# Performance work log

Hardware: AMD Instinct MI355X
Metric: run time of the kernel (lower is better)

Reference implementation:

```python
import jax, jax.numpy as jnp
import numpy as np

BETA = 0.05  # module hardcodes self.beta = 0.05 regardless of init arg
K = 4096
D = 512


def setup_inputs() -> dict:
    key = jax.random.key(0)
    k1, k2 = jax.random.split(key)
    latents = jax.random.normal(k1, (32, 1024, D), dtype=jnp.float32)
    # nn.Embedding weight init: normal_(mean=0.8, std=0.1)
    emb_weight = 0.8 + 0.1 * jax.random.normal(k2, (K, D), dtype=jnp.float32)
    return {"latents": latents, "emb_weight": emb_weight}


def reference(latents, emb_weight):
    B, S, Dm = latents.shape
    flat = latents.reshape(-1, Dm)  # [N, D]
    dist = (jnp.sum(flat * flat, axis=1, keepdims=True)
            + jnp.sum(emb_weight * emb_weight, axis=1)
            - 2.0 * jnp.matmul(flat, emb_weight.T))  # [N, K]
    inds = jnp.argmin(dist, axis=1)  # [N]
    quantized = emb_weight[inds].reshape(B, S, Dm)  # gather instead of one-hot matmul

    commitment_loss = jnp.mean((jax.lax.stop_gradient(quantized) - latents) ** 2)
    embedding_loss = jnp.mean((quantized - jax.lax.stop_gradient(latents)) ** 2)
    vq_loss = commitment_loss * BETA + embedding_loss

    # straight-through estimator
    quantized_st = latents + jax.lax.stop_gradient(quantized - latents)

    N = flat.shape[0]
    avg_probs = jnp.zeros((K,), dtype=latents.dtype).at[inds].add(1.0) / N
    perplexity = jnp.exp(-jnp.sum(avg_probs * jnp.log(avg_probs + 1e-10)))

    output_inds = inds.reshape(B, S)
    return (quantized_st, vq_loss, output_inds, emb_weight, perplexity)
```

## Files before the change

kernel.cpp:

```cpp
#include <hip/hip_runtime.h>
#include <cfloat>
#include <cmath>
#include <climits>
#include <cstdint>

#define N_ROWS   32768
#define D_DIM    512
#define K_CODES  4096

#define EPS_GAP  0.008f
#define CAND_WIN 0.02f
#define FLAG_CAP 12000

typedef short s16x8 __attribute__((ext_vector_type(8)));
typedef float f32x4 __attribute__((ext_vector_type(4)));


__device__ __forceinline__ short f2bf_rne(float x) {
    unsigned u = __float_as_uint(x);
    unsigned r = (u + 0x7fffu + ((u >> 16) & 1u)) >> 16;
    return (short)r;
}
__device__ __forceinline__ float bf2f(short b) {
    return __uint_as_float(((unsigned)(unsigned short)b) << 16);
}

__device__ __forceinline__ void gld16(const short* g, short* l) {
    __builtin_amdgcn_global_load_lds(
        reinterpret_cast<const __attribute__((address_space(1))) unsigned int*>(
            reinterpret_cast<uintptr_t>(g)),
        reinterpret_cast<__attribute__((address_space(3))) unsigned int*>(
            (unsigned int)(reinterpret_cast<uintptr_t>(l))),
        16, 0, 0);
}

__device__ __forceinline__ float np_block128_sq(const float* p) {
    float P[16];
    #pragma unroll
    for (int l = 0; l < 16; ++l) {
        float s0 = __fmul_rn(p[0 * 16 + l], p[0 * 16 + l]);
        float s1 = __fmul_rn(p[1 * 16 + l], p[1 * 16 + l]);
        float s2 = __fmul_rn(p[2 * 16 + l], p[2 * 16 + l]);
        float s3 = __fmul_rn(p[3 * 16 + l], p[3 * 16 + l]);
        float s4 = __fmul_rn(p[4 * 16 + l], p[4 * 16 + l]);
        float s5 = __fmul_rn(p[5 * 16 + l], p[5 * 16 + l]);
        float s6 = __fmul_rn(p[6 * 16 + l], p[6 * 16 + l]);
        float s7 = __fmul_rn(p[7 * 16 + l], p[7 * 16 + l]);
        float a01 = __fadd_rn(s0, s1);
        float a23 = __fadd_rn(s2, s3);
        float a45 = __fadd_rn(s4, s5);
        float a67 = __fadd_rn(s6, s7);
        P[l] = __fadd_rn(__fadd_rn(a01, a23), __fadd_rn(a45, a67));
    }
    float T3[8];
    #pragma unroll
    for (int k = 0; k < 8; ++k) T3[k] = __fadd_rn(P[k], P[k + 8]);
    float T6[4];
    #pragma unroll
    for (int k = 0; k < 4; ++k) T6[k] = __fadd_rn(T3[k], T3[k + 4]);
    return __fadd_rn(__fadd_rn(__fadd_rn(T6[0], T6[1]), T6[2]), T6[3]);
}
__device__ __forceinline__ float np_sum512_sq(const float* p) {
    float B0 = np_block128_sq(p);
    float B1 = np_block128_sq(p + 128);
    float B2 = np_block128_sq(p + 256);
    float B3 = np_block128_sq(p + 384);
    return __fadd_rn(__fadd_rn(B0, B1), __fadd_rn(B2, B3));
}

__global__ void vq_convert(const float* __restrict__ lat, const float* __restrict__ emb,
                           short* __restrict__ lat_hi, short* __restrict__ lat_lo,
                           short* __restrict__ emb_hi, short* __restrict__ emb_lo) {
    int i = blockIdx.x * 256 + threadIdx.x;
    const float* src; short *dh, *dl; size_t base;
    if (i < 2097152) { src = lat; dh = lat_hi; dl = lat_lo; base = (size_t)i * 8; }
    else             { src = emb; dh = emb_hi; dl = emb_lo; base = (size_t)(i - 2097152) * 8; }
    float4 a = *(const float4*)(src + base);
    float4 b = *(const float4*)(src + base + 4);
    float x[8] = {a.x, a.y, a.z, a.w, b.x, b.y, b.z, b.w};
    s16x8 hv, lv;
    #pragma unroll
    for (int j = 0; j < 8; ++j) {
        short h = f2bf_rne(x[j]);
        hv[j] = h;
        lv[j] = f2bf_rne(x[j] - bf2f(h));
    }
    *(s16x8*)(dh + base) = hv;
    *(s16x8*)(dl + base) = lv;
}

__global__ void vq_enorm(const float* __restrict__ emb, float* __restrict__ e_norm) {
    int item = blockIdx.x * 4 + (threadIdx.x >> 6);
    int lane = threadIdx.x & 63;
    const float4* s4 = (const float4*)(emb + (size_t)item * D_DIM);
    float4 a = s4[lane];
    float4 b = s4[64 + lane];
    float s = a.x * a.x + a.y * a.y + a.z * a.z + a.w * a.w
            + b.x * b.x + b.y * b.y + b.z * b.z + b.w * b.w;
    #pragma unroll
    for (int off = 32; off > 0; off >>= 1) s += __shfl_down(s, off);
    if (lane == 0) e_norm[item] = s;
}

__device__ __forceinline__ int kswz(int r) { return (r & 3) ^ ((r >> 2) & 3); }

#define BUFS 24576

__global__ __launch_bounds__(512, 2)
void vq_argmin_mfma(const short* __restrict__ Ah_g, const short* __restrict__ Al_g,
                    const short* __restrict__ Bh_g, const short* __restrict__ Bl_g,
                    const float* __restrict__ e_norm,
                    unsigned short* __restrict__ fidx,
                    int* __restrict__ flagcnt, int* __restrict__ flaglist)
{
    __shared__ short smem[2 * BUFS];

    const int tid = threadIdx.x;
    const int l   = tid & 63;
    const int wid = tid >> 6;
    const int wr  = wid >> 2;
    const int wc  = wid & 3;
    const int l15 = l & 15;
    const int lhi = l >> 4;
    const int row0 = blockIdx.x * 128;

    float best[16], sec[16];
    int   bidx[16];
    #pragma unroll
    for (int s = 0; s < 16; ++s) { best[s] = FLT_MAX; sec[s] = FLT_MAX; bidx[s] = 0; }

    int offA[4], offB[4];
    #pragma unroll
    for (int m = 0; m < 4; ++m) {
        int r = wr * 64 + m * 16 + l15;
        offA[m] = r * 32 + (lhi ^ kswz(r)) * 8;
    }
    #pragma unroll
    for (int n = 0; n < 4; ++n) {
        int r = wc * 64 + n * 16 + l15;
        offB[n] = r * 32 + (lhi ^ kswz(r)) * 8;
    }

    const int ar  = tid >> 2, asl = tid & 3;
    const size_t a_go0 = (size_t)(row0 + ar) * D_DIM + (asl ^ kswz(ar)) * 8;

    {
        gld16(Ah_g + a_go0, smem + tid * 8);
        gld16(Al_g + a_go0, smem + 4096 + tid * 8);
        #pragma unroll
        for (int jj = 0; jj < 2; ++jj) {
            int cc = jj * 512 + tid;
            int rr = cc >> 2, sll = cc & 3;
            size_t go = (size_t)rr * D_DIM + (sll ^ kswz(rr)) * 8;
            gld16(Bh_g + go, smem + 8192 + cc * 8);
            gld16(Bl_g + go, smem + 16384 + cc * 8);
        }
    }
    __syncthreads();

    f32x4 acc[4][4];
    #pragma unroll
    for (int m = 0; m < 4; ++m)
        #pragma unroll
        for (int n = 0; n < 4; ++n) acc[m][n] = (f32x4){0.f, 0.f, 0.f, 0.f};

    for (int s = 0; s < 256; ++s) {
        short* cur = smem + (s & 1) * BUFS;

        if (s < 255) {
            const int s1 = s + 1;
            const int k0 = (s1 & 15) * 32;
            const int cb0 = (s1 >> 4) * 256;
            short* nb = smem + ((s1 & 1)) * BUFS;
            gld16(Ah_g + a_go0 + k0, nb + tid * 8);
            gld16(Al_g + a_go0 + k0, nb + 4096 + tid * 8);
            #pragma unroll
            for (int jj = 0; jj < 2; ++jj) {
                int cc = jj * 512 + tid;
                int rr = cc >> 2, sll = cc & 3;
                size_t go = (size_t)(cb0 + rr) * D_DIM + k0 + (sll ^ kswz(rr)) * 8;
                gld16(Bh_g + go, nb + 8192 + cc * 8);
                gld16(Bl_g + go, nb + 16384 + cc * 8);
            }
        }

        s16x8 ah[4], al[4], bh[4], bl[4];
        #pragma unroll
        for (int m = 0; m < 4; ++m) {
            ah[m] = *(const s16x8*)(cur + offA[m]);
            al[m] = *(const s16x8*)(cur + 4096 + offA[m]);
        }
        #pragma unroll
        for (int n = 0; n < 4; ++n) {
            bh[n] = *(const s16x8*)(cur + 8192 + offB[n]);
            bl[n] = *(const s16x8*)(cur + 16384 + offB[n]);
        }

        #pragma unroll
        for (int m = 0; m < 4; ++m)
            #pragma unroll
            for (int n = 0; n < 4; ++n) {
                acc[m][n] = __builtin_amdgcn_mfma_f32_16x16x32_bf16(ah[m], bh[n], acc[m][n], 0, 0, 0);
                acc[m][n] = __builtin_amdgcn_mfma_f32_16x16x32_bf16(ah[m], bl[n], acc[m][n], 0, 0, 0);
                acc[m][n] = __builtin_amdgcn_mfma_f32_16x16x32_bf16(al[m], bh[n], acc[m][n], 0, 0, 0);
            }

        if ((s & 15) == 15) {
            const int cb0 = (s >> 4) * 256;
            #pragma unroll
            for (int n = 0; n < 4; ++n) {
                int c = cb0 + wc * 64 + n * 16 + l15;
                float en = e_norm[c];
                #pragma unroll
                for (int m = 0; m < 4; ++m)
                    #pragma unroll
                    for (int r = 0; r < 4; ++r) {
                        float dv = __fmaf_rn(-2.f, acc[m][n][r], en);
                        int si = m * 4 + r;
                        if (dv < best[si]) { sec[si] = best[si]; best[si] = dv; bidx[si] = c; }
                        else if (dv < sec[si]) sec[si] = dv;
                    }
            }
            #pragma unroll
            for (int m = 0; m < 4; ++m)
                #pragma unroll
                for (int n = 0; n < 4; ++n) acc[m][n] = (f32x4){0.f, 0.f, 0.f, 0.f};
        }

        __syncthreads();
    }

    #pragma unroll
    for (int s = 0; s < 16; ++s) {
        float v = best[s], sc = sec[s];
        int ix = bidx[s];
        #pragma unroll
        for (int off = 8; off > 0; off >>= 1) {
            float v2 = __shfl_xor(v, off);
            float s2 = __shfl_xor(sc, off);
            int   i2 = __shfl_xor(ix, off);
            float ns = fminf(fminf(sc, s2), fmaxf(v, v2));
            if (v2 < v || (v2 == v && i2 < ix)) { v = v2; ix = i2; }
            sc = ns;
        }
        best[s] = v; sec[s] = sc; bidx[s] = ix;
    }

    float* mb = (float*)smem;
    float* ms = mb + 512;
    int*   mi = (int*)(mb + 1024);
    if (l15 == 0) {
        #pragma unroll
        for (int m = 0; m < 4; ++m)
            #pragma unroll
            for (int r = 0; r < 4; ++r) {
                int s = m * 4 + r;
                int rowblk = wr * 64 + m * 16 + lhi * 4 + r;
                mb[wc * 128 + rowblk] = best[s];
                ms[wc * 128 + rowblk] = sec[s];
                mi[wc * 128 + rowblk] = bidx[s];
            }
    }
    __syncthreads();
    if (tid < 128) {
        float B = FLT_MAX, S = FLT_MAX;
        int I = 0;
        #pragma unroll
        for (int w = 0; w < 4; ++w) {
            float b = mb[w * 128 + tid], s = ms[w * 128 + tid];
            int i = mi[w * 128 + tid];
            if (b < B || (b == B && i < I)) { S = fminf(B, s); B = b; I = i; }
            else S = fminf(S, fminf(b, s));
        }
        int row = row0 + tid;
        fidx[row] = (unsigned short)I;
        if (S - B < EPS_GAP) {
            int p = atomicAdd(flagcnt, 1);
            if (p < FLAG_CAP) flaglist[p] = row;
        }
    }
}

#define FIXT 1024
#define NWAV 16
#define MAXC 128

__global__ __launch_bounds__(FIXT)
void vq_fixrow(const float* __restrict__ lat, const float* __restrict__ emb,
               const int* __restrict__ flagcnt, const int* __restrict__ flaglist,
               unsigned short* __restrict__ fidx)
{
    __shared__ float xs[D_DIM];
    __shared__ float dall[K_CODES];
    __shared__ float wmin_s[NWAV];
    __shared__ int   ccnt;
    __shared__ int   cands[MAXC];
    __shared__ float cd32[MAXC];

    const int t    = threadIdx.x;
    const int wave = t >> 6;
    const int lane = t & 63;
    int cnt = *flagcnt;
    if (cnt > FLAG_CAP) cnt = FLAG_CAP;

    for (int f = blockIdx.x; f < cnt; f += gridDim.x) {
        const int row = flaglist[f];
        __syncthreads();
        if (t < D_DIM) xs[t] = lat[(size_t)row * D_DIM + t];
        if (t == 0) ccnt = 0;
        __syncthreads();

        float x8[8];
        #pragma unroll
        for (int q = 0; q < 8; ++q) x8[q] = xs[lane * 8 + q];

        float lmin = FLT_MAX;
        for (int c = wave; c < K_CODES; c += 2 * NWAV) {
            const int c2 = c + NWAV;
            const float4* e4a = (const float4*)(emb + (size_t)c  * D_DIM);
            const float4* e4b = (const float4*)(emb + (size_t)c2 * D_DIM);
            float4 ea0 = e4a[lane * 2], ea1 = e4a[lane * 2 + 1];
            float4 eb0 = e4b[lane * 2], eb1 = e4b[lane * 2 + 1];

            float p0 = x8[0] - ea0.x, p1 = x8[1] - ea0.y;
            float p2 = x8[2] - ea0.z, p3 = x8[3] - ea0.w;
            float p4 = x8[4] - ea1.x, p5 = x8[5] - ea1.y;
            float p6 = x8[6] - ea1.z, p7 = x8[7] - ea1.w;
            float sA = __fmaf_rn(p0, p0, __fmaf_rn(p1, p1, __fmaf_rn(p2, p2, p3 * p3)));
            float sB = __fmaf_rn(p4, p4, __fmaf_rn(p5, p5, __fmaf_rn(p6, p6, p7 * p7)));
            float u = sA + sB;

            float q0 = x8[0] - eb0.x, q1 = x8[1] - eb0.y;
            float q2 = x8[2] - eb0.z, q3 = x8[3] - eb0.w;
            float q4 = x8[4] - eb1.x, q5 = x8[5] - eb1.y;
            float q6 = x8[6] - eb1.z, q7 = x8[7] - eb1.w;
            float tA = __fmaf_rn(q0, q0, __fmaf_rn(q1, q1, __fmaf_rn(q2, q2, q3 * q3)));
            float tB = __fmaf_rn(q4, q4, __fmaf_rn(q5, q5, __fmaf_rn(q6, q6, q7 * q7)));
            float v = tA + tB;

            #pragma unroll
            for (int off = 32; off > 0; off >>= 1) {
                u += __shfl_xor(u, off);
                v += __shfl_xor(v, off);
            }
            if (lane == 0) { dall[c] = u; dall[c2] = v; }
            lmin = fminf(lmin, fminf(u, v));
        }
        if (lane == 0) wmin_s[wave] = lmin;
        __syncthreads();

        float gmin = wmin_s[0];
        #pragma unroll
        for (int w = 1; w < NWAV; ++w) gmin = fminf(gmin, wmin_s[w]);
        const float thr = gmin + CAND_WIN;

        for (int c = t; c < K_CODES; c += FIXT) {
            if (dall[c] < thr) {
                int p = atomicAdd(&ccnt, 1);
                if (p < MAXC) cands[p] = c;
            }
        }
        __syncthreads();

        int nc = ccnt < MAXC ? ccnt : MAXC;
        if (t < nc) {
            int c = cands[t];
            const float* e = emb + (size_t)c * D_DIM;
            float t1 = np_sum512_sq(xs);
            float t2 = np_sum512_sq(e);
            float dot = 0.f;
            for (int k = 0; k < D_DIM; ++k)
                dot = __fmaf_rn(xs[k], e[k], dot);
            cd32[t] = __fsub_rn(__fadd_rn(t1, t2), __fmul_rn(2.f, dot));
        }
        __syncthreads();

        if (t == 0) {
            float bv = cd32[0]; int bx = cands[0];
            for (int w = 1; w < nc; ++w)
                if (cd32[w] < bv || (cd32[w] == bv && cands[w] < bx)) {
                    bv = cd32[w]; bx = cands[w];
                }
            fidx[row] = (unsigned short)bx;
        }
    }
}

__global__ void vq_gather(const float* __restrict__ lat, const float* __restrict__ emb,
                          const unsigned short* __restrict__ fidx,
                          float* __restrict__ out_q,
                          float* __restrict__ rowpart, int* __restrict__ hist) {
    int row  = blockIdx.x * 4 + (threadIdx.x >> 6);
    int lane = threadIdx.x & 63;
    int idx  = fidx[row];

    if (lane == 0) atomicAdd(&hist[idx], 1);

    const float4* e4 = (const float4*)(emb + (size_t)idx * D_DIM);
    const float4* x4 = (const float4*)(lat + (size_t)row * D_DIM);
    float4*       q4 = (float4*)(out_q + (size_t)row * D_DIM);

    float s = 0.f;
    #pragma unroll
    for (int i = 0; i < 2; ++i) {
        float4 e = e4[i * 64 + lane];
        float4 x = x4[i * 64 + lane];
        q4[i * 64 + lane] = e;
        float dx = e.x - x.x, dy = e.y - x.y, dz = e.z - x.z, dw = e.w - x.w;
        s += dx * dx + dy * dy + dz * dz + dw * dw;
    }
    #pragma unroll
    for (int off = 32; off > 0; off >>= 1) s += __shfl_down(s, off);
    if (lane == 0) rowpart[row] = s;
}

__global__ void vq_finalize(const float* __restrict__ rowpart, const int* __restrict__ hist,
                            float* __restrict__ out_loss, float* __restrict__ out_perp) {
    __shared__ float sdata[256];
    int t = threadIdx.x;

    float s = 0.f;
    for (int i = t; i < N_ROWS; i += 256) s += rowpart[i];
    sdata[t] = s;
    __syncthreads();
    for (int st = 128; st > 0; st >>= 1) {
        if (t < st) sdata[t] += sdata[t + st];
        __syncthreads();
    }
    if (t == 0) out_loss[0] = 1.05f * (sdata[0] / ((float)N_ROWS * (float)D_DIM));
    __syncthreads();

    float p = 0.f;
    for (int i = t; i < K_CODES; i += 256) {
        float pr = (float)hist[i] / (float)N_ROWS;
        p += pr * logf(pr + 1e-10f);
    }
    sdata[t] = p;
    __syncthreads();
    for (int st = 128; st > 0; st >>= 1) {
        if (t < st) sdata[t] += sdata[t + st];
        __syncthreads();
    }
    if (t == 0) out_perp[0] = expf(-sdata[0]);
}

__global__ void vq_inds(const unsigned short* __restrict__ fidx, float* __restrict__ out_inds) {
    int i = blockIdx.x * 1024 + threadIdx.x;
    out_inds[i] = (float)fidx[i];
}

extern "C" void kernel_launch(void* const* d_in, const int* in_sizes, int n_in,
                              void* d_out, int out_size, void* d_ws, size_t ws_size,
                              hipStream_t stream) {
    const float* lat = (const float*)d_in[0];
    const float* emb = (const float*)d_in[1];
    float* ob = (float*)d_out;

    short* emb_hi = (short*)(ob + 0);
    short* emb_lo = (short*)(ob + 1048576);
    short* lat_hi = (short*)(ob + 2097152);
    short* lat_lo = (short*)(ob + 10485760);
    float* e_norm = ob + 18874368;
    int*   flagcnt  = (int*)(ob + 18878464);
    int*   flaglist = (int*)(ob + 18878465);
    unsigned short* fidx = (unsigned short*)(ob + 18890496);
    int*   hist    = (int*)(ob + 16777220);
    float* rowpart = ob + 16781316;

    float* out_q    = ob;
    float* out_loss = ob + 16777216;
    float* out_inds = ob + 16777217;
    float* out_emb  = ob + 16809985;
    float* out_perp = ob + 18907137;

    hipMemsetAsync(flagcnt, 0, sizeof(int), stream);

    vq_convert<<<dim3(9216), dim3(256), 0, stream>>>(lat, emb, lat_hi, lat_lo, emb_hi, emb_lo);
    vq_enorm<<<dim3(1024), dim3(256), 0, stream>>>(emb, e_norm);

    vq_argmin_mfma<<<dim3(256), dim3(512), 0, stream>>>(lat_hi, lat_lo, emb_hi, emb_lo,
                                                        e_norm, fidx, flagcnt, flaglist);

    hipMemsetAsync(hist, 0, K_CODES * sizeof(int), stream);

    vq_fixrow<<<dim3(512), dim3(FIXT), 0, stream>>>(lat, emb, flagcnt, flaglist, fidx);

    vq_gather<<<dim3(N_ROWS / 4), dim3(256), 0, stream>>>(lat, emb, fidx, out_q, rowpart, hist);

    vq_finalize<<<dim3(1), dim3(256), 0, stream>>>(rowpart, hist, out_loss, out_perp);

    vq_inds<<<dim3(32), dim3(1024), 0, stream>>>(fidx, out_inds);

    hipMemcpyAsync(out_emb, emb, (size_t)K_CODES * D_DIM * sizeof(float),
                   hipMemcpyDeviceToDevice, stream);
}
```

Before: 845.9 us.

## Fuse latent bf16 split into argmin GEMM and split codebook across two blocks

Stops writing hi/lo bf16 copies of the latents to global memory. The argmin kernel now loads fp32 latents and splits them into hi/lo in registers while the next tile is prefetched. The tile grows to 256 rows with 1024 threads, and the codebook is split into two halves along a second grid dimension, followed by a small select kernel that merges the partial minima and flags close calls. Per-row running best/second values move from registers into shared memory and are updated after a shuffle reduction. This removes a large conversion pass and its traffic, at the cost of extra LDS traffic, more synchronisation, and occupancy pressure from the larger block.

```diff
diff --git a/kernel.cpp b/kernel.cpp
--- a/kernel.cpp
+++ b/kernel.cpp
@@ -68,15 +68,12 @@
     return __fadd_rn(__fadd_rn(B0, B1), __fadd_rn(B2, B3));
 }
 
-__global__ void vq_convert(const float* __restrict__ lat, const float* __restrict__ emb,
-                           short* __restrict__ lat_hi, short* __restrict__ lat_lo,
+__global__ void vq_convert(const float* __restrict__ emb,
                            short* __restrict__ emb_hi, short* __restrict__ emb_lo) {
     int i = blockIdx.x * 256 + threadIdx.x;
-    const float* src; short *dh, *dl; size_t base;
-    if (i < 2097152) { src = lat; dh = lat_hi; dl = lat_lo; base = (size_t)i * 8; }
-    else             { src = emb; dh = emb_hi; dl = emb_lo; base = (size_t)(i - 2097152) * 8; }
-    float4 a = *(const float4*)(src + base);
-    float4 b = *(const float4*)(src + base + 4);
+    size_t base = (size_t)i * 8;
+    float4 a = *(const float4*)(emb + base);
+    float4 b = *(const float4*)(emb + base + 4);
     float x[8] = {a.x, a.y, a.z, a.w, b.x, b.y, b.z, b.w};
     s16x8 hv, lv;
     #pragma unroll
@@ -85,8 +82,8 @@
         hv[j] = h;
         lv[j] = f2bf_rne(x[j] - bf2f(h));
     }
-    *(s16x8*)(dh + base) = hv;
-    *(s16x8*)(dl + base) = lv;
+    *(s16x8*)(emb_hi + base) = hv;
+    *(s16x8*)(emb_lo + base) = lv;
 }
 
 __global__ void vq_enorm(const float* __restrict__ emb, float* __restrict__ e_norm) {
@@ -104,16 +101,21 @@
 
 __device__ __forceinline__ int kswz(int r) { return (r & 3) ^ ((r >> 2) & 3); }
 
-#define BUFS 24576
-
-__global__ __launch_bounds__(512, 2)
-void vq_argmin_mfma(const short* __restrict__ Ah_g, const short* __restrict__ Al_g,
+#define BROWS 256
+#define BCOLS 256
+#define KHALF 2048
+#define BUFS2 32768
+
+__global__ __launch_bounds__(1024, 4)
+void vq_argmin_mfma(const float* __restrict__ lat,
                     const short* __restrict__ Bh_g, const short* __restrict__ Bl_g,
                     const float* __restrict__ e_norm,
-                    unsigned short* __restrict__ fidx,
-                    int* __restrict__ flagcnt, int* __restrict__ flaglist)
+                    float* __restrict__ pmin, unsigned short* __restrict__ pidx16)
 {
-    __shared__ short smem[2 * BUFS];
+    __shared__ short smem[2 * BUFS2];
+    __shared__ float pbest_s[4][256];
+    __shared__ float psec_s[4][256];
+    __shared__ int   pidx_s[4][256];
 
     const int tid = threadIdx.x;
     const int l   = tid & 63;
@@ -122,12 +124,12 @@
     const int wc  = wid & 3;
     const int l15 = l & 15;
     const int lhi = l >> 4;
-    const int row0 = blockIdx.x * 128;
-
-    float best[16], sec[16];
-    int   bidx[16];
-    #pragma unroll
-    for (int s = 0; s < 16; ++s) { best[s] = FLT_MAX; sec[s] = FLT_MAX; bidx[s] = 0; }
+    const int row0  = blockIdx.x * BROWS;
+    const int kbase = blockIdx.y * KHALF;
+
+    ((float*)pbest_s)[tid] = FLT_MAX;
+    ((float*)psec_s)[tid]  = FLT_MAX;
+    ((int*)pidx_s)[tid]    = 0;
 
     int offA[4], offB[4];
     #pragma unroll
@@ -137,24 +139,35 @@
     }
     #pragma unroll
     for (int n = 0; n < 4; ++n) {
-        int r = wc * 64 + n * 16 + l15;
-        offB[n] = r * 32 + (lhi ^ kswz(r)) * 8;
-    }
-
-    const int ar  = tid >> 2, asl = tid & 3;
-    const size_t a_go0 = (size_t)(row0 + ar) * D_DIM + (asl ^ kswz(ar)) * 8;
+        int c = wc * 64 + n * 16 + l15;
+        offB[n] = c * 32 + (lhi ^ kswz(c)) * 8;
+    }
+
+    const int ar = tid >> 2, asl = tid & 3;
+    const int achunk = asl ^ kswz(ar);
+    const size_t a_base = (size_t)(row0 + ar) * D_DIM + achunk * 8;
+    const int adst = ar * 32 + asl * 8;
+    const int br = tid >> 2, bsl = tid & 3;
+    const int bchunk = bsl ^ kswz(br);
+    const int bdst = tid * 8;
 
     {
-        gld16(Ah_g + a_go0, smem + tid * 8);
-        gld16(Al_g + a_go0, smem + 4096 + tid * 8);
-        #pragma unroll
-        for (int jj = 0; jj < 2; ++jj) {
-            int cc = jj * 512 + tid;
-            int rr = cc >> 2, sll = cc & 3;
-            size_t go = (size_t)rr * D_DIM + (sll ^ kswz(rr)) * 8;
-            gld16(Bh_g + go, smem + 8192 + cc * 8);
-            gld16(Bl_g + go, smem + 16384 + cc * 8);
-        }
+        size_t go = (size_t)(kbase + br) * D_DIM + bchunk * 8;
+        gld16(Bh_g + go, smem + 16384 + bdst);
+        gld16(Bl_g + go, smem + 24576 + bdst);
+        const float* p = lat + a_base;
+        float4 f0 = *(const float4*)p;
+        float4 f1 = *(const float4*)(p + 4);
+        float x[8] = {f0.x, f0.y, f0.z, f0.w, f1.x, f1.y, f1.z, f1.w};
+        s16x8 hv, lv;
+        #pragma unroll
+        for (int j = 0; j < 8; ++j) {
+            short h = f2bf_rne(x[j]);
+            hv[j] = h;
+            lv[j] = f2bf_rne(x[j] - bf2f(h));
+        }
+        *(s16x8*)(smem + adst) = hv;
+        *(s16x8*)(smem + 8192 + adst) = lv;
     }
     __syncthreads();
 
@@ -164,120 +177,132 @@
         #pragma unroll
         for (int n = 0; n < 4; ++n) acc[m][n] = (f32x4){0.f, 0.f, 0.f, 0.f};
 
-    for (int s = 0; s < 256; ++s) {
-        short* cur = smem + (s & 1) * BUFS;
-
-        if (s < 255) {
+    for (int s = 0; s < 128; ++s) {
+        short* cur = smem + (s & 1) * BUFS2;
+        short* nxt = smem + ((s & 1) ^ 1) * BUFS2;
+
+        float4 nf0, nf1;
+        if (s < 127) {
             const int s1 = s + 1;
             const int k0 = (s1 & 15) * 32;
-            const int cb0 = (s1 >> 4) * 256;
-            short* nb = smem + ((s1 & 1)) * BUFS;
-            gld16(Ah_g + a_go0 + k0, nb + tid * 8);
-            gld16(Al_g + a_go0 + k0, nb + 4096 + tid * 8);
-            #pragma unroll
-            for (int jj = 0; jj < 2; ++jj) {
-                int cc = jj * 512 + tid;
-                int rr = cc >> 2, sll = cc & 3;
-                size_t go = (size_t)(cb0 + rr) * D_DIM + k0 + (sll ^ kswz(rr)) * 8;
-                gld16(Bh_g + go, nb + 8192 + cc * 8);
-                gld16(Bl_g + go, nb + 16384 + cc * 8);
-            }
-        }
-
-        s16x8 ah[4], al[4], bh[4], bl[4];
+            const float* p = lat + a_base + k0;
+            nf0 = *(const float4*)p;
+            nf1 = *(const float4*)(p + 4);
+            size_t go = (size_t)(kbase + (s1 >> 4) * 256 + br) * D_DIM + k0 + bchunk * 8;
+            gld16(Bh_g + go, nxt + 16384 + bdst);
+            gld16(Bl_g + go, nxt + 24576 + bdst);
+        }
+
+        s16x8 ah[4], al[4];
         #pragma unroll
         for (int m = 0; m < 4; ++m) {
             ah[m] = *(const s16x8*)(cur + offA[m]);
-            al[m] = *(const s16x8*)(cur + 4096 + offA[m]);
+            al[m] = *(const s16x8*)(cur + 8192 + offA[m]);
         }
         #pragma unroll
         for (int n = 0; n < 4; ++n) {
-            bh[n] = *(const s16x8*)(cur + 8192 + offB[n]);
-            bl[n] = *(const s16x8*)(cur + 16384 + offB[n]);
-        }
-
-        #pragma unroll
-        for (int m = 0; m < 4; ++m)
+            s16x8 bh = *(const s16x8*)(cur + 16384 + offB[n]);
+            s16x8 bl = *(const s16x8*)(cur + 24576 + offB[n]);
+            #pragma unroll
+            for (int m = 0; m < 4; ++m) {
+                acc[m][n] = __builtin_amdgcn_mfma_f32_16x16x32_bf16(ah[m], bh, acc[m][n], 0, 0, 0);
+                acc[m][n] = __builtin_amdgcn_mfma_f32_16x16x32_bf16(ah[m], bl, acc[m][n], 0, 0, 0);
+                acc[m][n] = __builtin_amdgcn_mfma_f32_16x16x32_bf16(al[m], bh, acc[m][n], 0, 0, 0);
+            }
+        }
+
+        if ((s & 15) == 15) {
+            const int cb0 = kbase + (s >> 4) * 256;
+            float en[4];
+            int   cc[4];
             #pragma unroll
             for (int n = 0; n < 4; ++n) {
-                acc[m][n] = __builtin_amdgcn_mfma_f32_16x16x32_bf16(ah[m], bh[n], acc[m][n], 0, 0, 0);
-                acc[m][n] = __builtin_amdgcn_mfma_f32_16x16x32_bf16(ah[m], bl[n], acc[m][n], 0, 0, 0);
-                acc[m][n] = __builtin_amdgcn_mfma_f32_16x16x32_bf16(al[m], bh[n], acc[m][n], 0, 0, 0);
-            }
-
-        if ((s & 15) == 15) {
-            const int cb0 = (s >> 4) * 256;
-            #pragma unroll
-            for (int n = 0; n < 4; ++n) {
-                int c = cb0 + wc * 64 + n * 16 + l15;
-                float en = e_norm[c];
-                #pragma unroll
-                for (int m = 0; m < 4; ++m)
-                    #pragma unroll
-                    for (int r = 0; r < 4; ++r) {
-                        float dv = __fmaf_rn(-2.f, acc[m][n][r], en);
-                        int si = m * 4 + r;
-                        if (dv < best[si]) { sec[si] = best[si]; best[si] = dv; bidx[si] = c; }
-                        else if (dv < sec[si]) sec[si] = dv;
-                    }
+                cc[n] = cb0 + wc * 64 + n * 16 + l15;
+                en[n] = e_norm[cc[n]];
             }
             #pragma unroll
             for (int m = 0; m < 4; ++m)
                 #pragma unroll
+                for (int r = 0; r < 4; ++r) {
+                    float v = FLT_MAX, sc = FLT_MAX;
+                    int ii = 0;
+                    #pragma unroll
+                    for (int n = 0; n < 4; ++n) {
+                        float dv = __fmaf_rn(-2.f, acc[m][n][r], en[n]);
+                        if (dv < v) { sc = v; v = dv; ii = cc[n]; }
+                        else if (dv < sc) sc = dv;
+                    }
+                    #pragma unroll
+                    for (int off = 8; off > 0; off >>= 1) {
+                        float v2 = __shfl_xor(v, off);
+                        float s2 = __shfl_xor(sc, off);
+                        int   i2 = __shfl_xor(ii, off);
+                        float ns = fminf(fminf(sc, s2), fmaxf(v, v2));
+                        if (v2 < v || (v2 == v && i2 < ii)) { v = v2; ii = i2; }
+                        sc = ns;
+                    }
+                    if (l15 == 0) {
+                        int rb = wr * 64 + m * 16 + lhi * 4 + r;
+                        float ob = pbest_s[wc][rb];
+                        float os = psec_s[wc][rb];
+                        float nsec = fminf(fminf(os, sc), fmaxf(ob, v));
+                        if (v < ob) { pbest_s[wc][rb] = v; pidx_s[wc][rb] = ii; }
+                        psec_s[wc][rb] = nsec;
+                    }
+                }
+            #pragma unroll
+            for (int m = 0; m < 4; ++m)
+                #pragma unroll
                 for (int n = 0; n < 4; ++n) acc[m][n] = (f32x4){0.f, 0.f, 0.f, 0.f};
         }
 
-        __syncthreads();
-    }
-
-    #pragma unroll
-    for (int s = 0; s < 16; ++s) {
-        float v = best[s], sc = sec[s];
-        int ix = bidx[s];
-        #pragma unroll
-        for (int off = 8; off > 0; off >>= 1) {
-            float v2 = __shfl_xor(v, off);
-            float s2 = __shfl_xor(sc, off);
-            int   i2 = __shfl_xor(ix, off);
-            float ns = fminf(fminf(sc, s2), fmaxf(v, v2));
-            if (v2 < v || (v2 == v && i2 < ix)) { v = v2; ix = i2; }
-            sc = ns;
-        }
-        best[s] = v; sec[s] = sc; bidx[s] = ix;
-    }
-
-    float* mb = (float*)smem;
-    float* ms = mb + 512;
-    int*   mi = (int*)(mb + 1024);
-    if (l15 == 0) {
-        #pragma unroll
-        for (int m = 0; m < 4; ++m)
+        if (s < 127) {
+            float x[8] = {nf0.x, nf0.y, nf0.z, nf0.w, nf1.x, nf1.y, nf1.z, nf1.w};
+            s16x8 hv, lv;
             #pragma unroll
-            for (int r = 0; r < 4; ++r) {
-                int s = m * 4 + r;
-                int rowblk = wr * 64 + m * 16 + lhi * 4 + r;
-                mb[wc * 128 + rowblk] = best[s];
-                ms[wc * 128 + rowblk] = sec[s];
-                mi[wc * 128 + rowblk] = bidx[s];
+            for (int j = 0; j < 8; ++j) {
+                short h = f2bf_rne(x[j]);
+                hv[j] = h;
+                lv[j] = f2bf_rne(x[j] - bf2f(h));
             }
-    }
-    __syncthreads();
-    if (tid < 128) {
+            *(s16x8*)(nxt + adst) = hv;
+            *(s16x8*)(nxt + 8192 + adst) = lv;
+        }
+        __syncthreads();
+    }
+
+    if (tid < 256) {
         float B = FLT_MAX, S = FLT_MAX;
         int I = 0;
         #pragma unroll
         for (int w = 0; w < 4; ++w) {
-            float b = mb[w * 128 + tid], s = ms[w * 128 + tid];
-            int i = mi[w * 128 + tid];
+            float b = pbest_s[w][tid], s = psec_s[w][tid];
+            int i = pidx_s[w][tid];
             if (b < B || (b == B && i < I)) { S = fminf(B, s); B = b; I = i; }
             else S = fminf(S, fminf(b, s));
         }
         int row = row0 + tid;
-        fidx[row] = (unsigned short)I;
-        if (S - B < EPS_GAP) {
-            int p = atomicAdd(flagcnt, 1);
-            if (p < FLAG_CAP) flaglist[p] = row;
-        }
+        pmin[blockIdx.y * N_ROWS + row] = B;
+        unsigned short pk = (unsigned short)I;
+        if (S - B < EPS_GAP) pk |= 0x8000;
+        pidx16[blockIdx.y * N_ROWS + row] = pk;
+    }
+}
+
+__global__ void vq_select(const float* __restrict__ pmin,
+                          const unsigned short* __restrict__ pidx16,
+                          unsigned short* __restrict__ fidx,
+                          int* __restrict__ flagcnt, int* __restrict__ flaglist) {
+    int row = blockIdx.x * 256 + threadIdx.x;
+    float v0 = pmin[row], v1 = pmin[N_ROWS + row];
+    unsigned p0 = pidx16[row], p1 = pidx16[N_ROWS + row];
+    int i0 = p0 & 0xFFF, i1 = p1 & 0xFFF;
+    int bi = (v1 < v0) ? i1 : i0;
+    fidx[row] = (unsigned short)bi;
+    bool fl = ((p0 | p1) & 0x8000u) != 0 || fabsf(v0 - v1) < EPS_GAP;
+    if (fl) {
+        int p = atomicAdd(flagcnt, 1);
+        if (p < FLAG_CAP) flaglist[p] = row;
     }
 }
 
@@ -458,14 +483,14 @@
 
     short* emb_hi = (short*)(ob + 0);
     short* emb_lo = (short*)(ob + 1048576);
-    short* lat_hi = (short*)(ob + 2097152);
-    short* lat_lo = (short*)(ob + 10485760);
-    float* e_norm = ob + 18874368;
-    int*   flagcnt  = (int*)(ob + 18878464);
-    int*   flaglist = (int*)(ob + 18878465);
-    unsigned short* fidx = (unsigned short*)(ob + 18890496);
-    int*   hist    = (int*)(ob + 16777220);
-    float* rowpart = ob + 16781316;
+    float* pmin   = ob + 2097152;
+    unsigned short* pidx16 = (unsigned short*)(ob + 2162688);
+    float* e_norm = ob + 2195456;
+    int*   flagcnt  = (int*)(ob + 2199552);
+    int*   flaglist = (int*)(ob + 2199553);
+    unsigned short* fidx = (unsigned short*)(ob + 16810000);
+    int*   hist    = (int*)(ob + 16826384);
+    float* rowpart = ob + 16830480;
 
     float* out_q    = ob;
     float* out_loss = ob + 16777216;
@@ -474,14 +499,16 @@
     float* out_perp = ob + 18907137;
 
     hipMemsetAsync(flagcnt, 0, sizeof(int), stream);
-
-    vq_convert<<<dim3(9216), dim3(256), 0, stream>>>(lat, emb, lat_hi, lat_lo, emb_hi, emb_lo);
+    hipMemsetAsync(hist, 0, K_CODES * sizeof(int), stream);
+
+    vq_convert<<<dim3(1024), dim3(256), 0, stream>>>(emb, emb_hi, emb_lo);
     vq_enorm<<<dim3(1024), dim3(256), 0, stream>>>(emb, e_norm);
 
-    vq_argmin_mfma<<<dim3(256), dim3(512), 0, stream>>>(lat_hi, lat_lo, emb_hi, emb_lo,
-                                                        e_norm, fidx, flagcnt, flaglist);
-
-    hipMemsetAsync(hist, 0, K_CODES * sizeof(int), stream);
+    vq_argmin_mfma<<<dim3(N_ROWS / BROWS, 2), dim3(1024), 0, stream>>>(
+        lat, emb_hi, emb_lo, e_norm, pmin, pidx16);
+
+    vq_select<<<dim3(N_ROWS / 256), dim3(256), 0, stream>>>(pmin, pidx16,
+                                                            fidx, flagcnt, flaglist);
 
     vq_fixrow<<<dim3(512), dim3(FIXT), 0, stream>>>(lat, emb, flagcnt, flaglist, fidx);
 
```

Result: slower. 914.1 us (+8.1%).
